# Kernel tuning notes

Hardware: AMD Instinct MI355X
Metric: run time of the kernel (lower is better)

The kernel has to match this reference:

```python
import jax, jax.numpy as jnp
import numpy as np

N = 4096      # atoms
K = 5         # atoms gathered per cell (top_k in put_atoms_in_cells)
M = 8         # neighbors kept per atom
NBR = 26      # neighbor cells per cell (9+9+8)

def _grid():
    # get_cells: box [-10,10) step 1 Angstrom -> 20^3 = 8000 cells
    g = jnp.arange(-10.0, 10.0, 1.0)
    X = jnp.stack(jnp.meshgrid(g, g, g))       # (3,20,20,20), tf.meshgrid default 'xy'
    return jnp.transpose(X).reshape(-1, 3)      # (8000,3)

def _sqdist(a, b):
    # ||a_i - b_j||^2 via expansion; avoids (A,B,3) intermediate
    return (jnp.sum(a * a, 1)[:, None] + jnp.sum(b * b, 1)[None, :] - 2.0 * (a @ b.T))

def _neighbor_list(coords):
    cells = _grid()                              # (n_cells, 3)
    # put_atoms_in_cells: tf.nn.top_k(norm, k) -> k LARGEST norms (faithful to source)
    d_ca = _sqdist(cells, coords)                # (n_cells, N)
    _, atoms_in_cells = jax.lax.top_k(d_ca, K)   # (n_cells, K)
    # get_cells_for_atoms: top_k(-norm, 1) -> closest cell per atom
    d_ac = _sqdist(coords, cells)                # (N, n_cells)
    cells_for_atoms = jnp.argmin(d_ac, axis=1)   # (N,)
    # compute_neighbor_cells: top_k(norm, 26) (faithful to source)
    d_cc = _sqdist(cells, cells)                 # (n_cells, n_cells)
    _, nbr_cells = jax.lax.top_k(d_cc, NBR)      # (n_cells, 26)
    nbr_cells_atom = nbr_cells[cells_for_atoms]  # (N, 26)
    nbr_inds = atoms_in_cells[nbr_cells_atom]    # (N, 26, K)
    nbr_coords = coords[nbr_inds]                # (N, 26, K, 3)
    dists = jnp.sum((coords[:, None, None, :] - nbr_coords) ** 2, axis=-1)
    dists = dists.reshape(N, NBR * K)            # (N, 130)
    _, locs = jax.lax.top_k(dists, M)            # top_k(dists, M) as in source
    flat = nbr_inds.reshape(N, NBR * K)
    return jnp.take_along_axis(flat, locs, axis=1)   # (N, M) atom indices

def _energy(coords, vdw, weights, nrot, nbr):
    # d_ij = r_ij - R_i - R_j
    diff = coords[:, None, :] - coords[nbr]      # (N, M, 3)
    r = jnp.sqrt(jnp.sum(diff * diff, axis=-1) + 1e-12)
    d = r - vdw[:, None] - vdw[nbr]
    g1 = jnp.exp(-(d / 0.5) ** 2)
    g2 = jnp.exp(-((d - 3.0) / 2.0) ** 2)
    rep = jnp.where(d < 0.0, d * d, 0.0)
    hyd = jnp.where(d < 0.5, 1.0, jnp.where(d < 1.5, 1.5 - d, 0.0))
    hb = jnp.where(d < -0.7, 1.0, jnp.where(d < 0.0, -d / 0.7, 0.0))
    hval = (weights[0] * g1 + weights[1] * g2 + weights[2] * rep
            + weights[3] * hyd + weights[4] * hb)
    f = jnp.where(d < 8.0, hval, 0.0)            # cutoff at 8 Angstrom
    c = jnp.sum(f)
    return c / (1.0 + weights[5] * nrot[0])      # g(c, Nrot)

def setup_inputs() -> dict:
    key = jax.random.key(0)
    k1, k2, k3 = jax.random.split(key, 3)
    coords = jax.random.uniform(k1, (N, 3), jnp.float32, -10.0, 10.0)
    vdw = jax.random.uniform(k2, (N,), jnp.float32, 1.0, 2.0)
    weights = 0.3 * jax.random.normal(k3, (6,), jnp.float32)
    nrot = 8.0 * jnp.ones((1,), jnp.float32)
    return {"coords": coords, "vdw": vdw, "weights": weights, "nrot": nrot}

def reference(coords, vdw, weights, nrot):
    nbr = _neighbor_list(coords)
    return _energy(coords, vdw, weights, nrot, nbr)
```

## Files before the change

kernel.cpp:

```cpp
#include <hip/hip_runtime.h>
#include <stdint.h>

#define NATOMS 4096
#define NCELLS 8000
#define KTOP 5
#define MNBR 8
#define NBRC 26
#define HBINS 217
#define LSTMAX 512

__device__ __forceinline__ unsigned long long umax64(unsigned long long a, unsigned long long b) {
    return a > b ? a : b;
}
__device__ __forceinline__ unsigned long long umin64(unsigned long long a, unsigned long long b) {
    return a < b ? a : b;
}

__device__ __forceinline__ void cell_coords_i(int m, int& x, int& y, int& z) {
    int a = m / 400;
    int r = m - a * 400;
    int b = r / 20;
    int c = r - b * 20;
    x = b - 10; y = c - 10; z = a - 10;
}

__global__ __launch_bounds__(256) void kcellsforatoms(const float* __restrict__ coords,
                                                      int* __restrict__ cellsForAtoms,
                                                      int* __restrict__ neededFlag) {
    {
        int z = blockIdx.x * 8 + threadIdx.x;
        if (threadIdx.x < 8 && z < NCELLS) neededFlag[z] = 0;
    }
    const int wid = threadIdx.x >> 6;
    const int lane = threadIdx.x & 63;
    const int atom = blockIdx.x * 4 + wid;

    float ax = coords[atom * 3], ay = coords[atom * 3 + 1], az = coords[atom * 3 + 2];
    float sa = __fadd_rn(__fadd_rn(__fmul_rn(ax, ax), __fmul_rn(ay, ay)), __fmul_rn(az, az));

    int fx = (int)floorf(ax), fy = (int)floorf(ay), fz = (int)floorf(az);
    int vx = min(9, max(-10, fx - 1 + (lane & 3)));
    int vy = min(9, max(-10, fy - 1 + ((lane >> 2) & 3)));
    int vz = min(9, max(-10, fz - 1 + (lane >> 4)));
    int m = (vz + 10) * 400 + (vx + 10) * 20 + (vy + 10);

    float cx = (float)vx, cy = (float)vy, cz = (float)vz;
    float scell = (float)(vx * vx + vy * vy + vz * vz);
    float dot = __fadd_rn(__fadd_rn(__fmul_rn(ax, cx), __fmul_rn(ay, cy)), __fmul_rn(az, cz));
    float val = __fsub_rn(__fadd_rn(sa, scell), __fmul_rn(2.0f, dot));
    unsigned long long key = ((unsigned long long)__float_as_uint(val) << 32) | (unsigned int)m;

    for (int off = 32; off > 0; off >>= 1)
        key = umin64(key, (unsigned long long)__shfl_xor((long long)key, off));
    if (lane == 0) cellsForAtoms[atom] = (int)(key & 0xFFFFFFFFull);
}

__global__ __launch_bounds__(256) void knbr2(const int* __restrict__ cellsForAtoms,
                                             int* __restrict__ nbrTable,
                                             int* __restrict__ neededFlag) {
    const int ci = cellsForAtoms[blockIdx.x];
    const int t = threadIdx.x;
    const int lane = t & 63;

    int xi, yi, zi;
    cell_coords_i(ci, xi, yi, zi);
    const int Lx = max(xi + 10, 9 - xi);
    const int Ly = max(yi + 10, 9 - yi);
    const int Lz = max(zi + 10, 9 - zi);
    const int lo = (Lx - 2) * (Lx - 2) + (Ly - 2) * (Ly - 2) + (Lz - 2) * (Lz - 2);

    __shared__ uint32_t h[HBINS];
    __shared__ int lst[LSTMAX];
    __shared__ int sV, cnt;

    if (t < HBINS) h[t] = 0;
    if (t == 0) cnt = 0;
    __syncthreads();

#pragma unroll
    for (int col = 0; col < 2; ++col) {
        int p = t + 256 * col;
        if (p < 400) {
            int bb = p / 20, cc = p - bb * 20;
            int dxv = xi - (bb - 10), dyv = yi - (cc - 10);
            int Dbc = dxv * dxv + dyv * dyv;
            int R = lo - Dbc;
            int aLoEnd = 19, aHiStart = 20;
            if (R > 0) {
                int t0 = (int)ceilf(sqrtf((float)R));
                if ((t0 - 1) * (t0 - 1) >= R) --t0;
                if (t0 * t0 < R) ++t0;
                aLoEnd = min(19, zi + 10 - t0);
                aHiStart = max(0, zi + 10 + t0);
            }
            for (int a = 0; a <= aLoEnd; ++a) {
                int dzv = zi - (a - 10);
                int d = Dbc + dzv * dzv;
                atomicAdd(&h[d - lo], 1u);
            }
            for (int a = aHiStart; a < 20; ++a) {
                int dzv = zi - (a - 10);
                int d = Dbc + dzv * dzv;
                atomicAdd(&h[d - lo], 1u);
            }
        }
    }
    __syncthreads();

    if (t < 64) {
        int c4[4];
        int cnt4 = 0;
#pragma unroll
        for (int k = 0; k < 4; ++k) {
            int b = (HBINS - 1) - (t * 4 + k);
            c4[k] = (b >= 0) ? (int)h[b] : 0;
            cnt4 += c4[k];
        }
        int incl = cnt4;
        for (int off = 1; off < 64; off <<= 1) {
            int v = __shfl_up(incl, off);
            if (lane >= off) incl += v;
        }
        int P = incl - cnt4;
        if (P < NBRC && incl >= NBRC) {
            int run = P;
#pragma unroll
            for (int k = 0; k < 4; ++k) {
                run += c4[k];
                if (run >= NBRC) { sV = lo + (HBINS - 1) - (t * 4 + k); break; }
            }
        }
    }
    __syncthreads();
    const int V = sV;

#pragma unroll
    for (int col = 0; col < 2; ++col) {
        int p = t + 256 * col;
        if (p < 400) {
            int bb = p / 20, cc = p - bb * 20;
            int dxv = xi - (bb - 10), dyv = yi - (cc - 10);
            int Dbc = dxv * dxv + dyv * dyv;
            int R = V - Dbc;
            int aLoEnd = 19, aHiStart = 20;
            if (R > 0) {
                int t0 = (int)ceilf(sqrtf((float)R));
                if ((t0 - 1) * (t0 - 1) >= R) --t0;
                if (t0 * t0 < R) ++t0;
                aLoEnd = min(19, zi + 10 - t0);
                aHiStart = max(0, zi + 10 + t0);
            }
            for (int a = 0; a <= aLoEnd; ++a) {
                int dzv = zi - (a - 10);
                int d = Dbc + dzv * dzv;
                int j = a * 400 + p;
                int q = atomicAdd(&cnt, 1);
                if (q < LSTMAX) lst[q] = (d << 13) | (8191 - j);
            }
            for (int a = aHiStart; a < 20; ++a) {
                int dzv = zi - (a - 10);
                int d = Dbc + dzv * dzv;
                int j = a * 400 + p;
                int q = atomicAdd(&cnt, 1);
                if (q < LSTMAX) lst[q] = (d << 13) | (8191 - j);
            }
        }
    }
    __syncthreads();

    int n = min(cnt, LSTMAX);
    if (t < 64) {
        for (int base = 0; base < n; base += 64) {
            int idx = base + t;
            int key = (idx < n) ? lst[idx] : -1;
            int rank = 0;
            for (int m = 0; m < n; ++m) rank += (lst[m] > key) ? 1 : 0;
            if (idx < n && rank < NBRC) {
                int j = 8191 - (key & 8191);
                nbrTable[ci * NBRC + rank] = j;
                neededFlag[j] = 1;
            }
        }
    }
}

__global__ __launch_bounds__(256) void katoms2(const float* __restrict__ coords,
                                               const int* __restrict__ neededFlag,
                                               int* __restrict__ atomsInCells) {
    const int i = blockIdx.x;
    if (!neededFlag[i]) return;
    __shared__ unsigned long long redB[4];
    const int t = threadIdx.x;
    const int lane = t & 63, wv = t >> 6;

    int xi_, yi_, zi_;
    cell_coords_i(i, xi_, yi_, zi_);
    const float cx = (float)xi_, cy = (float)yi_, cz = (float)zi_;
    const float scell = (float)(xi_ * xi_ + yi_ * yi_ + zi_ * zi_);

    unsigned long long keys[16];
#pragma unroll
    for (int s = 0; s < 16; ++s) {
        int j = t + 256 * s;
        float ax = coords[j * 3], ay = coords[j * 3 + 1], az = coords[j * 3 + 2];
        float sa = __fadd_rn(__fadd_rn(__fmul_rn(ax, ax), __fmul_rn(ay, ay)), __fmul_rn(az, az));
        float dot = __fadd_rn(__fadd_rn(__fmul_rn(cx, ax), __fmul_rn(cy, ay)), __fmul_rn(cz, az));
        float val = __fsub_rn(__fadd_rn(scell, sa), __fmul_rn(2.0f, dot));
        keys[s] = ((unsigned long long)__float_as_uint(val) << 32) | (unsigned int)(4095 - j);
    }

    for (int r = 0; r < KTOP; ++r) {
        unsigned long long best = 0ull;
#pragma unroll
        for (int s = 0; s < 16; ++s) best = umax64(best, keys[s]);
        for (int off = 32; off > 0; off >>= 1)
            best = umax64(best, (unsigned long long)__shfl_xor((long long)best, off));
        if (lane == 0) redB[wv] = best;
        __syncthreads();
        unsigned long long wbest = umax64(umax64(redB[0], redB[1]), umax64(redB[2], redB[3]));
        if (t == 0) atomsInCells[i * KTOP + r] = 4095 - (int)(wbest & 0xFFFFFFFFull);
#pragma unroll
        for (int s = 0; s < 16; ++s) if (keys[s] == wbest) keys[s] = 0ull;
        __syncthreads();
    }
}

__global__ __launch_bounds__(256) void kenergy(const float* __restrict__ coords,
                                               const float* __restrict__ vdw,
                                               const float* __restrict__ weights,
                                               const int* __restrict__ nbrTable,
                                               const int* __restrict__ atomsInCells,
                                               const int* __restrict__ cellsForAtoms,
                                               float* __restrict__ partials) {
    const int wid = threadIdx.x >> 6;
    const int lane = threadIdx.x & 63;
    const int i = blockIdx.x * 4 + wid;

    const float xi = coords[i * 3], yi = coords[i * 3 + 1], zi = coords[i * 3 + 2];
    const int ci = cellsForAtoms[i];

    int cand[3];
    unsigned long long keys[3];
#pragma unroll
    for (int s = 0; s < 3; ++s) {
        int p = lane + 64 * s;
        cand[s] = -1;
        keys[s] = 0ull;
        if (p < NBRC * KTOP) {
            int cellSlot = p / KTOP;
            int atomSlot = p - cellSlot * KTOP;
            int nc = nbrTable[ci * NBRC + cellSlot];
            int j = atomsInCells[nc * KTOP + atomSlot];
            cand[s] = j;
            float dx = __fsub_rn(xi, coords[j * 3]);
            float dy = __fsub_rn(yi, coords[j * 3 + 1]);
            float dz = __fsub_rn(zi, coords[j * 3 + 2]);
            float dist = __fadd_rn(__fadd_rn(__fmul_rn(dx, dx), __fmul_rn(dy, dy)), __fmul_rn(dz, dz));
            keys[s] = ((unsigned long long)__float_as_uint(dist) << 8) | (unsigned int)(255 - p);
        }
    }

    const float w0 = weights[0], w1 = weights[1], w2 = weights[2];
    const float w3 = weights[3], w4 = weights[4];
    const float vi = vdw[i];

    float esum = 0.0f;
    for (int r = 0; r < MNBR; ++r) {
        unsigned long long best = umax64(umax64(keys[0], keys[1]), keys[2]);
        for (int off = 32; off > 0; off >>= 1)
            best = umax64(best, (unsigned long long)__shfl_xor((long long)best, off));

        int p = 255 - (int)(best & 0xFFull);
        int slot = p >> 6;
        int owner = p & 63;
        int jsel = (slot == 0) ? cand[0] : (slot == 1) ? cand[1] : cand[2];
        int j = __shfl(jsel, owner);
        float dist = __uint_as_float((unsigned int)(best >> 8));

#pragma unroll
        for (int s = 0; s < 3; ++s) if (keys[s] == best) keys[s] = 0ull;

        float rr = __fsqrt_rn(__fadd_rn(dist, 1e-12f));
        float d = __fsub_rn(__fsub_rn(rr, vi), vdw[j]);
        float t1 = __fdiv_rn(d, 0.5f);
        float g1 = expf(-__fmul_rn(t1, t1));
        float t2 = __fdiv_rn(__fsub_rn(d, 3.0f), 2.0f);
        float g2 = expf(-__fmul_rn(t2, t2));
        float rep = (d < 0.0f) ? __fmul_rn(d, d) : 0.0f;
        float hyd = (d < 0.5f) ? 1.0f : ((d < 1.5f) ? __fsub_rn(1.5f, d) : 0.0f);
        float hb = (d < -0.7f) ? 1.0f : ((d < 0.0f) ? __fdiv_rn(-d, 0.7f) : 0.0f);
        float hval = __fadd_rn(__fadd_rn(__fadd_rn(__fadd_rn(
                         __fmul_rn(w0, g1), __fmul_rn(w1, g2)),
                         __fmul_rn(w2, rep)), __fmul_rn(w3, hyd)), __fmul_rn(w4, hb));
        float f = (d < 8.0f) ? hval : 0.0f;
        esum = __fadd_rn(esum, f);
    }
    if (lane == 0) partials[i] = esum;
}

__global__ __launch_bounds__(256) void kreduce(const float* __restrict__ partials,
                                               const float* __restrict__ weights,
                                               const float* __restrict__ nrot,
                                               float* __restrict__ out) {
    __shared__ float red[256];
    const int t = threadIdx.x;
    float s = 0.0f;
    for (int k = 0; k < NATOMS / 256; ++k) s = __fadd_rn(s, partials[t + 256 * k]);
    red[t] = s;
    __syncthreads();
    for (int off = 128; off > 0; off >>= 1) {
        if (t < off) red[t] = __fadd_rn(red[t], red[t + off]);
        __syncthreads();
    }
    if (t == 0) out[0] = __fdiv_rn(red[0], __fadd_rn(1.0f, __fmul_rn(weights[5], nrot[0])));
}

extern "C" void kernel_launch(void* const* d_in, const int* in_sizes, int n_in,
                              void* d_out, int out_size, void* d_ws, size_t ws_size,
                              hipStream_t stream) {
    const float* coords  = (const float*)d_in[0];
    const float* vdw     = (const float*)d_in[1];
    const float* weights = (const float*)d_in[2];
    const float* nrot    = (const float*)d_in[3];
    float* out = (float*)d_out;

    int* nbrTable      = (int*)d_ws;
    int* atomsInCells  = nbrTable + NCELLS * NBRC;
    int* cellsForAtoms = atomsInCells + NCELLS * KTOP;
    int* neededFlag    = cellsForAtoms + NATOMS;
    float* partials    = (float*)(neededFlag + NCELLS);

    kcellsforatoms<<<NATOMS / 4, 256, 0, stream>>>(coords, cellsForAtoms, neededFlag);
    knbr2<<<NATOMS, 256, 0, stream>>>(cellsForAtoms, nbrTable, neededFlag);
    katoms2<<<NCELLS, 256, 0, stream>>>(coords, neededFlag, atomsInCells);
    kenergy<<<NATOMS / 4, 256, 0, stream>>>(coords, vdw, weights, nbrTable,
                                            atomsInCells, cellsForAtoms, partials);
    kreduce<<<1, 256, 0, stream>>>(partials, weights, nrot, out);
}
```

Before: 44.22 us.

## Fuse cell assignment into neighbor kernel and fold final reduction into energy

Cuts the launch sequence from five kernels to three. The per-atom closest-cell search now runs in the first wave of the neighbor-cell kernel, and its result passes through shared memory. The final reduction becomes an extra block in the energy kernel. That block spins on per-block acquire/release flags, which the atoms kernel resets each call, before summing the partials. The in-kernel zeroing of neededFlag is dropped and the check becomes `!= 1`. Flags can therefore go stale across calls, causing extra cell work, and the spin-wait depends on all producer blocks being resident or scheduled.

```diff
diff --git a/kernel.cpp b/kernel.cpp
--- a/kernel.cpp
+++ b/kernel.cpp
@@ -24,58 +24,55 @@
     x = b - 10; y = c - 10; z = a - 10;
 }
 
-__global__ __launch_bounds__(256) void kcellsforatoms(const float* __restrict__ coords,
-                                                      int* __restrict__ cellsForAtoms,
-                                                      int* __restrict__ neededFlag) {
-    {
-        int z = blockIdx.x * 8 + threadIdx.x;
-        if (threadIdx.x < 8 && z < NCELLS) neededFlag[z] = 0;
-    }
-    const int wid = threadIdx.x >> 6;
-    const int lane = threadIdx.x & 63;
-    const int atom = blockIdx.x * 4 + wid;
-
-    float ax = coords[atom * 3], ay = coords[atom * 3 + 1], az = coords[atom * 3 + 2];
-    float sa = __fadd_rn(__fadd_rn(__fmul_rn(ax, ax), __fmul_rn(ay, ay)), __fmul_rn(az, az));
-
-    int fx = (int)floorf(ax), fy = (int)floorf(ay), fz = (int)floorf(az);
-    int vx = min(9, max(-10, fx - 1 + (lane & 3)));
-    int vy = min(9, max(-10, fy - 1 + ((lane >> 2) & 3)));
-    int vz = min(9, max(-10, fz - 1 + (lane >> 4)));
-    int m = (vz + 10) * 400 + (vx + 10) * 20 + (vy + 10);
-
-    float cx = (float)vx, cy = (float)vy, cz = (float)vz;
-    float scell = (float)(vx * vx + vy * vy + vz * vz);
-    float dot = __fadd_rn(__fadd_rn(__fmul_rn(ax, cx), __fmul_rn(ay, cy)), __fmul_rn(az, cz));
-    float val = __fsub_rn(__fadd_rn(sa, scell), __fmul_rn(2.0f, dot));
-    unsigned long long key = ((unsigned long long)__float_as_uint(val) << 32) | (unsigned int)m;
-
-    for (int off = 32; off > 0; off >>= 1)
-        key = umin64(key, (unsigned long long)__shfl_xor((long long)key, off));
-    if (lane == 0) cellsForAtoms[atom] = (int)(key & 0xFFFFFFFFull);
-}
-
-__global__ __launch_bounds__(256) void knbr2(const int* __restrict__ cellsForAtoms,
-                                             int* __restrict__ nbrTable,
-                                             int* __restrict__ neededFlag) {
-    const int ci = cellsForAtoms[blockIdx.x];
+__global__ __launch_bounds__(256) void k1_cells_nbr(const float* __restrict__ coords,
+                                                    int* __restrict__ cellsForAtoms,
+                                                    int* __restrict__ nbrTable,
+                                                    int* __restrict__ neededFlag) {
+    const int atom = blockIdx.x;
     const int t = threadIdx.x;
     const int lane = t & 63;
 
+    __shared__ int sCi;
+    __shared__ uint32_t h[HBINS];
+    __shared__ int lst[LSTMAX];
+    __shared__ int sV, cnt;
+
+    if (t < HBINS) h[t] = 0;
+    if (t == 0) cnt = 0;
+
+    if (t < 64) {
+        float ax = coords[atom * 3], ay = coords[atom * 3 + 1], az = coords[atom * 3 + 2];
+        float sa = __fadd_rn(__fadd_rn(__fmul_rn(ax, ax), __fmul_rn(ay, ay)), __fmul_rn(az, az));
+
+        int fx = (int)floorf(ax), fy = (int)floorf(ay), fz = (int)floorf(az);
+        int vx = min(9, max(-10, fx - 1 + (lane & 3)));
+        int vy = min(9, max(-10, fy - 1 + ((lane >> 2) & 3)));
+        int vz = min(9, max(-10, fz - 1 + (lane >> 4)));
+        int m = (vz + 10) * 400 + (vx + 10) * 20 + (vy + 10);
+
+        float cx = (float)vx, cy = (float)vy, cz = (float)vz;
+        float scell = (float)(vx * vx + vy * vy + vz * vz);
+        float dot = __fadd_rn(__fadd_rn(__fmul_rn(ax, cx), __fmul_rn(ay, cy)), __fmul_rn(az, cz));
+        float val = __fsub_rn(__fadd_rn(sa, scell), __fmul_rn(2.0f, dot));
+        unsigned long long key = ((unsigned long long)__float_as_uint(val) << 32) | (unsigned int)m;
+
+        for (int off = 32; off > 0; off >>= 1)
+            key = umin64(key, (unsigned long long)__shfl_xor((long long)key, off));
+        if (lane == 0) {
+            int c = (int)(key & 0xFFFFFFFFull);
+            cellsForAtoms[atom] = c;
+            sCi = c;
+        }
+    }
+    __syncthreads();
+
+    const int ci = sCi;
     int xi, yi, zi;
     cell_coords_i(ci, xi, yi, zi);
     const int Lx = max(xi + 10, 9 - xi);
     const int Ly = max(yi + 10, 9 - yi);
     const int Lz = max(zi + 10, 9 - zi);
     const int lo = (Lx - 2) * (Lx - 2) + (Ly - 2) * (Ly - 2) + (Lz - 2) * (Lz - 2);
-
-    __shared__ uint32_t h[HBINS];
-    __shared__ int lst[LSTMAX];
-    __shared__ int sV, cnt;
-
-    if (t < HBINS) h[t] = 0;
-    if (t == 0) cnt = 0;
-    __syncthreads();
 
 #pragma unroll
     for (int col = 0; col < 2; ++col) {
@@ -95,13 +92,11 @@
             }
             for (int a = 0; a <= aLoEnd; ++a) {
                 int dzv = zi - (a - 10);
-                int d = Dbc + dzv * dzv;
-                atomicAdd(&h[d - lo], 1u);
+                atomicAdd(&h[Dbc + dzv * dzv - lo], 1u);
             }
             for (int a = aHiStart; a < 20; ++a) {
                 int dzv = zi - (a - 10);
-                int d = Dbc + dzv * dzv;
-                atomicAdd(&h[d - lo], 1u);
+                atomicAdd(&h[Dbc + dzv * dzv - lo], 1u);
             }
         }
     }
@@ -184,11 +179,13 @@
     }
 }
 
-__global__ __launch_bounds__(256) void katoms2(const float* __restrict__ coords,
-                                               const int* __restrict__ neededFlag,
-                                               int* __restrict__ atomsInCells) {
+__global__ __launch_bounds__(256) void k2_atoms(const float* __restrict__ coords,
+                                                const int* __restrict__ neededFlag,
+                                                int* __restrict__ atomsInCells,
+                                                int* __restrict__ flagDone) {
     const int i = blockIdx.x;
-    if (!neededFlag[i]) return;
+    if (threadIdx.x == 0 && i < 1024) flagDone[i] = 0;
+    if (neededFlag[i] != 1) return;
     __shared__ unsigned long long redB[4];
     const int t = threadIdx.x;
     const int lane = t & 63, wv = t >> 6;
@@ -225,15 +222,42 @@
     }
 }
 
-__global__ __launch_bounds__(256) void kenergy(const float* __restrict__ coords,
-                                               const float* __restrict__ vdw,
-                                               const float* __restrict__ weights,
-                                               const int* __restrict__ nbrTable,
-                                               const int* __restrict__ atomsInCells,
-                                               const int* __restrict__ cellsForAtoms,
-                                               float* __restrict__ partials) {
-    const int wid = threadIdx.x >> 6;
-    const int lane = threadIdx.x & 63;
+__global__ __launch_bounds__(256) void k3_energy_red(const float* __restrict__ coords,
+                                                     const float* __restrict__ vdw,
+                                                     const float* __restrict__ weights,
+                                                     const float* __restrict__ nrot,
+                                                     const int* __restrict__ nbrTable,
+                                                     const int* __restrict__ atomsInCells,
+                                                     const int* __restrict__ cellsForAtoms,
+                                                     float* __restrict__ partials,
+                                                     int* __restrict__ flagDone,
+                                                     float* __restrict__ out) {
+    __shared__ float red[256];
+    const int t = threadIdx.x;
+
+    if (blockIdx.x == 1024) {
+        for (int k = 0; k < 4; ++k) {
+            int f = t * 4 + k;
+            while (__hip_atomic_load(&flagDone[f], __ATOMIC_ACQUIRE,
+                                     __HIP_MEMORY_SCOPE_AGENT) != 1) {
+                __builtin_amdgcn_s_sleep(8);
+            }
+        }
+        __syncthreads();
+        float s = 0.0f;
+        for (int k = 0; k < NATOMS / 256; ++k) s = __fadd_rn(s, partials[t + 256 * k]);
+        red[t] = s;
+        __syncthreads();
+        for (int off = 128; off > 0; off >>= 1) {
+            if (t < off) red[t] = __fadd_rn(red[t], red[t + off]);
+            __syncthreads();
+        }
+        if (t == 0) out[0] = __fdiv_rn(red[0], __fadd_rn(1.0f, __fmul_rn(weights[5], nrot[0])));
+        return;
+    }
+
+    const int wid = t >> 6;
+    const int lane = t & 63;
     const int i = blockIdx.x * 4 + wid;
 
     const float xi = coords[i * 3], yi = coords[i * 3 + 1], zi = coords[i * 3 + 2];
@@ -296,23 +320,13 @@
         esum = __fadd_rn(esum, f);
     }
     if (lane == 0) partials[i] = esum;
-}
-
-__global__ __launch_bounds__(256) void kreduce(const float* __restrict__ partials,
-                                               const float* __restrict__ weights,
-                                               const float* __restrict__ nrot,
-                                               float* __restrict__ out) {
-    __shared__ float red[256];
-    const int t = threadIdx.x;
-    float s = 0.0f;
-    for (int k = 0; k < NATOMS / 256; ++k) s = __fadd_rn(s, partials[t + 256 * k]);
-    red[t] = s;
-    __syncthreads();
-    for (int off = 128; off > 0; off >>= 1) {
-        if (t < off) red[t] = __fadd_rn(red[t], red[t + off]);
-        __syncthreads();
-    }
-    if (t == 0) out[0] = __fdiv_rn(red[0], __fadd_rn(1.0f, __fmul_rn(weights[5], nrot[0])));
+
+    __syncthreads();
+    if (t == 0) {
+        __threadfence();
+        __hip_atomic_store(&flagDone[blockIdx.x], 1, __ATOMIC_RELEASE,
+                           __HIP_MEMORY_SCOPE_AGENT);
+    }
 }
 
 extern "C" void kernel_launch(void* const* d_in, const int* in_sizes, int n_in,
@@ -328,12 +342,12 @@
     int* atomsInCells  = nbrTable + NCELLS * NBRC;
     int* cellsForAtoms = atomsInCells + NCELLS * KTOP;
     int* neededFlag    = cellsForAtoms + NATOMS;
-    float* partials    = (float*)(neededFlag + NCELLS);
-
-    kcellsforatoms<<<NATOMS / 4, 256, 0, stream>>>(coords, cellsForAtoms, neededFlag);
-    knbr2<<<NATOMS, 256, 0, stream>>>(cellsForAtoms, nbrTable, neededFlag);
-    katoms2<<<NCELLS, 256, 0, stream>>>(coords, neededFlag, atomsInCells);
-    kenergy<<<NATOMS / 4, 256, 0, stream>>>(coords, vdw, weights, nbrTable,
-                                            atomsInCells, cellsForAtoms, partials);
-    kreduce<<<1, 256, 0, stream>>>(partials, weights, nrot, out);
-}
+    int* flagDone      = neededFlag + NCELLS;
+    float* partials    = (float*)(flagDone + 1024);
+
+    k1_cells_nbr<<<NATOMS, 256, 0, stream>>>(coords, cellsForAtoms, nbrTable, neededFlag);
+    k2_atoms<<<NCELLS, 256, 0, stream>>>(coords, neededFlag, atomsInCells, flagDone);
+    k3_energy_red<<<1025, 256, 0, stream>>>(coords, vdw, weights, nrot, nbrTable,
+                                            atomsInCells, cellsForAtoms, partials,
+                                            flagDone, out);
+}
```

Result: slower. 65.65 us (+48.5%).
